# Optimization experiments

Hardware: AMD Instinct MI355X
Metric: run time of the kernel (lower is better)

Reference implementation:

```python
import jax, jax.numpy as jnp
import numpy as np

FILT, HOP, N_MELS, SR, FMIN, FMAX = 1024, 256, 80, 16000, 0.0, 8000.0
CUTOFF = FILT // 2 + 1  # 513


def _hann_periodic(n):
    t = np.arange(n)
    return 0.5 - 0.5 * np.cos(2.0 * np.pi * t / n)


def _hz_to_mel(f):
    # librosa slaney scale (htk=False)
    f = np.asarray(f, dtype=np.float64)
    f_sp = 200.0 / 3.0
    min_log_hz = 1000.0
    min_log_mel = min_log_hz / f_sp
    logstep = np.log(6.4) / 27.0
    return np.where(f >= min_log_hz,
                    min_log_mel + np.log(np.maximum(f, 1e-10) / min_log_hz) / logstep,
                    f / f_sp)


def _mel_to_hz(m):
    m = np.asarray(m, dtype=np.float64)
    f_sp = 200.0 / 3.0
    min_log_hz = 1000.0
    min_log_mel = min_log_hz / f_sp
    logstep = np.log(6.4) / 27.0
    return np.where(m >= min_log_mel,
                    min_log_hz * np.exp(logstep * (m - min_log_mel)),
                    m * f_sp)


def _mel_filterbank(sr, n_fft, n_mels, fmin, fmax):
    # librosa.filters.mel with norm='slaney', htk=False
    fftfreqs = np.linspace(0.0, sr / 2.0, n_fft // 2 + 1)
    mel_f = _mel_to_hz(np.linspace(_hz_to_mel(fmin), _hz_to_mel(fmax), n_mels + 2))
    fdiff = np.diff(mel_f)
    ramps = mel_f[:, None] - fftfreqs[None, :]
    lower = -ramps[:-2] / fdiff[:-1, None]
    upper = ramps[2:] / fdiff[1:, None]
    weights = np.maximum(0.0, np.minimum(lower, upper))
    enorm = 2.0 / (mel_f[2:n_mels + 2] - mel_f[:n_mels])  # slaney normalization
    weights *= enorm[:, None]
    return weights.astype(np.float32)  # [n_mels, n_fft//2+1]


def _forward_basis(n_fft):
    # windowed real/imag DFT rows, as in STFT.__init__
    fourier = np.fft.fft(np.eye(n_fft))
    basis = np.vstack([fourier[:CUTOFF].real, fourier[:CUTOFF].imag]).astype(np.float32)
    basis *= _hann_periodic(n_fft).astype(np.float32)[None, :]
    return basis  # [2*CUTOFF, n_fft] = [1026, 1024]


def setup_inputs() -> dict:
    key = jax.random.key(0)
    y = jax.random.normal(key, (16, 524288), dtype=jnp.float32)
    forward_basis = jnp.asarray(_forward_basis(FILT))
    mel_basis = jnp.asarray(_mel_filterbank(SR, FILT, N_MELS, FMIN, FMAX))
    return {"y": y, "forward_basis": forward_basis, "mel_basis": mel_basis}


def reference(y, forward_basis, mel_basis):
    # STFT.transform: reflect pad by n_fft//2 then conv1d with DFT basis, stride=hop
    yp = jnp.pad(y, ((0, 0), (FILT // 2, FILT // 2)), mode='reflect')[:, None, :]  # [B,1,T+1024]
    ft = jax.lax.conv_general_dilated(
        yp, forward_basis[:, None, :], window_strides=(HOP,), padding='VALID',
        dimension_numbers=('NCH', 'OIH', 'NCH'))  # [B, 1026, n_frames]
    real, imag = ft[:, :CUTOFF, :], ft[:, CUTOFF:, :]
    magnitude = jnp.sqrt(real * real + imag * imag)  # [B, 513, n_frames]
    mel = jnp.einsum('mf,bft->bmt', mel_basis, magnitude)  # [B, 80, n_frames]
    return jnp.log(jnp.maximum(mel, 1e-5))
```

## Files before the change

kernel.cpp:

```cpp
#include <hip/hip_runtime.h>
#include <math.h>

#define HOP     256
#define CUTOFF  513
#define NMELS   80
#define BATCH   16
#define LEN     524288
#define NFRAMES 2049
#define NFFT    1024
#define KW      48
#define WSTRIDE 49
#define TBLK    16

#define ZIDX(i) ((i) + ((i) >> 4))

__device__ __forceinline__ float2 cmul(float2 a, float2 b) {
    return make_float2(a.x * b.x - a.y * b.y, a.x * b.y + a.y * b.x);
}

__global__ void setup_tables(float* __restrict__ tw, float* __restrict__ win) {
    int i = blockIdx.x * blockDim.x + threadIdx.x;
    if (i < NFFT / 2) {
        double th = -2.0 * M_PI * (double)i / (double)NFFT;
        tw[2 * i]     = (float)cos(th);
        tw[2 * i + 1] = (float)sin(th);
    }
    if (i < NFFT) {
        double th = 2.0 * M_PI * (double)i / (double)NFFT;
        win[i] = (float)(0.5 - 0.5 * cos(th));
    }
}

__global__ __launch_bounds__(256) void mel_pack(const float* __restrict__ melw,
                                                int* __restrict__ kstart,
                                                float* __restrict__ wpack) {
    __shared__ int smin;
    const int m = blockIdx.x;
    if (threadIdx.x == 0) smin = CUTOFF;
    __syncthreads();
    const float* row = melw + m * CUTOFF;
    int local = CUTOFF;
    for (int k = threadIdx.x; k < CUTOFF; k += 256)
        if (row[k] > 0.0f && k < local) local = k;
    atomicMin(&smin, local);
    __syncthreads();
    int ks = smin;
    if (ks >= CUTOFF) ks = 0;
    if (threadIdx.x == 0) kstart[m] = ks;
    for (int j = threadIdx.x; j < KW; j += 256) {
        int k = ks + j;
        wpack[m * KW + j] = (k < CUTOFF) ? row[k] : 0.0f;
    }
}

__global__ __launch_bounds__(256) void stft_mel(const float* __restrict__ y,
                                                const float* __restrict__ tw,
                                                const float* __restrict__ win,
                                                const int* __restrict__ kstart,
                                                const float* __restrict__ wpack,
                                                float* __restrict__ out) {
    __shared__ float2 z[NFFT + NFFT / 16];
    __shared__ float  mag0[576];
    __shared__ float  mag1[576];
    __shared__ float  wl[NMELS * WSTRIDE];
    __shared__ float  melbuf[NMELS][TBLK + 1];
    __shared__ int    ksl[NMELS];
    const int tid   = threadIdx.x;
    const int tbase = blockIdx.x * TBLK;
    const int b     = blockIdx.y;
    const float* yb = y + (size_t)b * LEN;
    const float2* twg = (const float2*)tw;

    float2 w1r[4], w2r[4], w3r[4];
    #pragma unroll
    for (int st = 0; st < 4; ++st) {
        const int L   = 1 << (8 - 2 * st);
        const int s   = 1 << (2 * st);
        const int off = tid & (L - 1);
        float2 wa = twg[off * s];
        float2 wb = twg[2 * off * s];
        w1r[st] = wa; w2r[st] = wb; w3r[st] = cmul(wa, wb);
    }
    float wreg[4];
    #pragma unroll
    for (int q = 0; q < 4; ++q) wreg[q] = win[tid + 256 * q];
    int r4;
    {
        int x = tid, r = 0;
        #pragma unroll
        for (int d4 = 0; d4 < 4; ++d4) { r = (r << 2) | (x & 3); x >>= 2; }
        r4 = r;
    }

    for (int i = tid; i < NMELS * KW; i += 256)
        wl[(i / KW) * WSTRIDE + (i % KW)] = wpack[i];
    if (tid < NMELS) ksl[tid] = kstart[tid];
    if (tid < 63) { mag0[CUTOFF + tid] = 0.0f; mag1[CUTOFF + tid] = 0.0f; }

    #pragma unroll 1
    for (int p = 0; p < TBLK / 2; ++p) {
        const int t0 = tbase + 2 * p;
        const int s0 = t0 * HOP - NFFT / 2;

        float2 e[4];
        #pragma unroll
        for (int q = 0; q < 4; ++q) {
            int praw = s0 + tid + 256 * q;
            int p0 = praw;
            p0 = p0 < 0 ? -p0 : p0;  p0 = p0 >= LEN ? 2 * LEN - 2 - p0 : p0;
            int p1 = praw + HOP;
            p1 = p1 < 0 ? -p1 : p1;  p1 = p1 >= LEN ? 2 * LEN - 2 - p1 : p1;
            e[q] = make_float2(wreg[q] * yb[p0], wreg[q] * yb[p1]);
        }
        {
            float2 t0v = make_float2(e[0].x + e[2].x, e[0].y + e[2].y);
            float2 t1v = make_float2(e[0].x - e[2].x, e[0].y - e[2].y);
            float2 t2v = make_float2(e[1].x + e[3].x, e[1].y + e[3].y);
            float2 t3v = make_float2(e[1].x - e[3].x, e[1].y - e[3].y);
            float2 mit3 = make_float2(t3v.y, -t3v.x);
            float2 B0 = make_float2(t0v.x + t2v.x,  t0v.y + t2v.y);
            float2 B2 = make_float2(t0v.x - t2v.x,  t0v.y - t2v.y);
            float2 B1 = make_float2(t1v.x + mit3.x, t1v.y + mit3.y);
            float2 B3 = make_float2(t1v.x - mit3.x, t1v.y - mit3.y);
            z[ZIDX(tid)]        = B0;
            z[ZIDX(tid + 256)]  = cmul(B1, w1r[0]);
            z[ZIDX(tid + 512)]  = cmul(B2, w2r[0]);
            z[ZIDX(tid + 768)]  = cmul(B3, w3r[0]);
        }
        __syncthreads();

        #pragma unroll
        for (int st = 1; st < 4; ++st) {
            const int L   = 1 << (8 - 2 * st);
            const int off = tid & (L - 1);
            const int i0  = ((tid & ~(L - 1)) << 2) | off;

            float2 a  = z[ZIDX(i0)];
            float2 bb = z[ZIDX(i0 + L)];
            float2 c  = z[ZIDX(i0 + 2 * L)];
            float2 d  = z[ZIDX(i0 + 3 * L)];

            float2 t0v = make_float2(a.x + c.x,  a.y + c.y);
            float2 t1v = make_float2(a.x - c.x,  a.y - c.y);
            float2 t2v = make_float2(bb.x + d.x, bb.y + d.y);
            float2 t3v = make_float2(bb.x - d.x, bb.y - d.y);
            float2 mit3 = make_float2(t3v.y, -t3v.x);

            float2 B0 = make_float2(t0v.x + t2v.x,  t0v.y + t2v.y);
            float2 B2 = make_float2(t0v.x - t2v.x,  t0v.y - t2v.y);
            float2 B1 = make_float2(t1v.x + mit3.x, t1v.y + mit3.y);
            float2 B3 = make_float2(t1v.x - mit3.x, t1v.y - mit3.y);

            z[ZIDX(i0)]         = B0;
            z[ZIDX(i0 + L)]     = cmul(B1, w1r[st]);
            z[ZIDX(i0 + 2 * L)] = cmul(B2, w2r[st]);
            z[ZIDX(i0 + 3 * L)] = cmul(B3, w3r[st]);
            __syncthreads();
        }

        {
            const int i0 = tid * 4;
            float2 a  = z[ZIDX(i0)];
            float2 bb = z[ZIDX(i0 + 1)];
            float2 c  = z[ZIDX(i0 + 2)];
            float2 d  = z[ZIDX(i0 + 3)];

            float2 t0v = make_float2(a.x + c.x,  a.y + c.y);
            float2 t1v = make_float2(a.x - c.x,  a.y - c.y);
            float2 t2v = make_float2(bb.x + d.x, bb.y + d.y);
            float2 t3v = make_float2(bb.x - d.x, bb.y - d.y);
            float2 mit3 = make_float2(t3v.y, -t3v.x);

            float2 B0 = make_float2(t0v.x + t2v.x,  t0v.y + t2v.y);
            float2 B2 = make_float2(t0v.x - t2v.x,  t0v.y - t2v.y);
            float2 B1 = make_float2(t1v.x + mit3.x, t1v.y + mit3.y);
            float2 B3 = make_float2(t1v.x - mit3.x, t1v.y - mit3.y);

            __syncthreads();
            z[ZIDX(r4)]        = B0;
            z[ZIDX(r4 + 256)]  = B1;
            z[ZIDX(r4 + 512)]  = B2;
            z[ZIDX(r4 + 768)]  = B3;
            __syncthreads();
        }

        for (int k = tid; k <= NFFT / 2; k += 256) {
            int nk = (NFFT - k) & (NFFT - 1);
            float2 Zk = z[ZIDX(k)], Zn = z[ZIDX(nk)];
            float f0r = 0.5f * (Zk.x + Zn.x);
            float f0i = 0.5f * (Zk.y - Zn.y);
            float f1r = 0.5f * (Zk.y + Zn.y);
            float f1i = 0.5f * (Zn.x - Zk.x);
            mag0[k] = sqrtf(f0r * f0r + f0i * f0i);
            mag1[k] = sqrtf(f1r * f1r + f1i * f1i);
        }
        __syncthreads();

        if (tid < NMELS) {
            const int m = tid;
            const float* wrow = &wl[m * WSTRIDE];
            const int ks = ksl[m];
            const float* m0 = &mag0[ks];
            const float* m1 = &mag1[ks];
            float acc0 = 0.0f, acc1 = 0.0f;
            #pragma unroll
            for (int j = 0; j < KW; ++j) {
                float w = wrow[j];
                acc0 += w * m0[j];
                acc1 += w * m1[j];
            }
            melbuf[m][2 * p]     = logf(fmaxf(acc0, 1e-5f));
            melbuf[m][2 * p + 1] = logf(fmaxf(acc1, 1e-5f));
        }
    }
    __syncthreads();

    for (int o = tid; o < NMELS * TBLK; o += 256) {
        int m = o >> 4;
        int j = o & (TBLK - 1);
        int t = tbase + j;
        if (t < NFRAMES)
            out[((size_t)b * NMELS + m) * NFRAMES + t] = melbuf[m][j];
    }
}

extern "C" void kernel_launch(void* const* d_in, const int* in_sizes, int n_in,
                              void* d_out, int out_size, void* d_ws, size_t ws_size,
                              hipStream_t stream) {
    const float* y    = (const float*)d_in[0];
    const float* melw = (const float*)d_in[2];
    float* out = (float*)d_out;

    float* tw     = (float*)d_ws;
    float* win    = tw + NFFT;
    int*   kstart = (int*)(win + NFFT);
    float* wpack  = (float*)(kstart + 128);

    setup_tables<<<4, 256, 0, stream>>>(tw, win);
    mel_pack<<<NMELS, 256, 0, stream>>>(melw, kstart, wpack);

    dim3 g((NFRAMES + TBLK - 1) / TBLK, BATCH);
    stft_mel<<<g, 256, 0, stream>>>(y, tw, win, kstart, wpack, out);
}
```

Measured before the change: 173.7 us.

## Prefetch next frame samples, use wave-local LDS fences, shrink mel width

```diff
diff --git a/kernel.cpp b/kernel.cpp
--- a/kernel.cpp
+++ b/kernel.cpp
@@ -8,11 +8,16 @@
 #define LEN     524288
 #define NFRAMES 2049
 #define NFFT    1024
-#define KW      48
-#define WSTRIDE 49
+#define KW      40
+#define WSTRIDE 41
 #define TBLK    16
+#define NPAIRS  (TBLK / 2)
+#define MAGPAD  (CUTOFF + KW - 1)
 
 #define ZIDX(i) ((i) + ((i) >> 4))
+
+#define BARRIER_LDS()    asm volatile("s_waitcnt lgkmcnt(0)\n\ts_barrier" ::: "memory")
+#define FENCE_WAVE_LDS() asm volatile("s_waitcnt lgkmcnt(0)" ::: "memory")
 
 __device__ __forceinline__ float2 cmul(float2 a, float2 b) {
     return make_float2(a.x * b.x - a.y * b.y, a.x * b.y + a.y * b.x);
@@ -60,8 +65,8 @@
                                                 const float* __restrict__ wpack,
                                                 float* __restrict__ out) {
     __shared__ float2 z[NFFT + NFFT / 16];
-    __shared__ float  mag0[576];
-    __shared__ float  mag1[576];
+    __shared__ float  mag0[MAGPAD];
+    __shared__ float  mag1[MAGPAD];
     __shared__ float  wl[NMELS * WSTRIDE];
     __shared__ float  melbuf[NMELS][TBLK + 1];
     __shared__ int    ksl[NMELS];
@@ -83,7 +88,7 @@
     }
     float wreg[4];
     #pragma unroll
-    for (int q = 0; q < 4; ++q) wreg[q] = win[tid + 256 * q];
+    for (int q = 0; q < 4; ++q) wreg[q] = 0.5f * win[tid + 256 * q];
     int r4;
     {
         int x = tid, r = 0;
@@ -95,14 +100,11 @@
     for (int i = tid; i < NMELS * KW; i += 256)
         wl[(i / KW) * WSTRIDE + (i % KW)] = wpack[i];
     if (tid < NMELS) ksl[tid] = kstart[tid];
-    if (tid < 63) { mag0[CUTOFF + tid] = 0.0f; mag1[CUTOFF + tid] = 0.0f; }
-
-    #pragma unroll 1
-    for (int p = 0; p < TBLK / 2; ++p) {
-        const int t0 = tbase + 2 * p;
-        const int s0 = t0 * HOP - NFFT / 2;
-
-        float2 e[4];
+    if (tid < KW - 1) { mag0[CUTOFF + tid] = 0.0f; mag1[CUTOFF + tid] = 0.0f; }
+
+    float pre[8];
+    {
+        const int s0 = tbase * HOP - NFFT / 2;
         #pragma unroll
         for (int q = 0; q < 4; ++q) {
             int praw = s0 + tid + 256 * q;
@@ -110,9 +112,18 @@
             p0 = p0 < 0 ? -p0 : p0;  p0 = p0 >= LEN ? 2 * LEN - 2 - p0 : p0;
             int p1 = praw + HOP;
             p1 = p1 < 0 ? -p1 : p1;  p1 = p1 >= LEN ? 2 * LEN - 2 - p1 : p1;
-            e[q] = make_float2(wreg[q] * yb[p0], wreg[q] * yb[p1]);
-        }
+            pre[2 * q]     = yb[p0];
+            pre[2 * q + 1] = yb[p1];
+        }
+    }
+
+    #pragma unroll 1
+    for (int p = 0; p < NPAIRS; ++p) {
         {
+            float2 e[4];
+            #pragma unroll
+            for (int q = 0; q < 4; ++q)
+                e[q] = make_float2(wreg[q] * pre[2 * q], wreg[q] * pre[2 * q + 1]);
             float2 t0v = make_float2(e[0].x + e[2].x, e[0].y + e[2].y);
             float2 t1v = make_float2(e[0].x - e[2].x, e[0].y - e[2].y);
             float2 t2v = make_float2(e[1].x + e[3].x, e[1].y + e[3].y);
@@ -127,7 +138,21 @@
             z[ZIDX(tid + 512)]  = cmul(B2, w2r[0]);
             z[ZIDX(tid + 768)]  = cmul(B3, w3r[0]);
         }
-        __syncthreads();
+        BARRIER_LDS();
+
+        if (p + 1 < NPAIRS) {
+            const int s0n = (tbase + 2 * (p + 1)) * HOP - NFFT / 2;
+            #pragma unroll
+            for (int q = 0; q < 4; ++q) {
+                int praw = s0n + tid + 256 * q;
+                int p0 = praw;
+                p0 = p0 < 0 ? -p0 : p0;  p0 = p0 >= LEN ? 2 * LEN - 2 - p0 : p0;
+                int p1 = praw + HOP;
+                p1 = p1 < 0 ? -p1 : p1;  p1 = p1 >= LEN ? 2 * LEN - 2 - p1 : p1;
+                pre[2 * q]     = yb[p0];
+                pre[2 * q + 1] = yb[p1];
+            }
+        }
 
         #pragma unroll
         for (int st = 1; st < 4; ++st) {
@@ -155,7 +180,7 @@
             z[ZIDX(i0 + L)]     = cmul(B1, w1r[st]);
             z[ZIDX(i0 + 2 * L)] = cmul(B2, w2r[st]);
             z[ZIDX(i0 + 3 * L)] = cmul(B3, w3r[st]);
-            __syncthreads();
+            FENCE_WAVE_LDS();
         }
 
         {
@@ -176,25 +201,25 @@
             float2 B1 = make_float2(t1v.x + mit3.x, t1v.y + mit3.y);
             float2 B3 = make_float2(t1v.x - mit3.x, t1v.y - mit3.y);
 
-            __syncthreads();
+            BARRIER_LDS();
             z[ZIDX(r4)]        = B0;
             z[ZIDX(r4 + 256)]  = B1;
             z[ZIDX(r4 + 512)]  = B2;
             z[ZIDX(r4 + 768)]  = B3;
-            __syncthreads();
+            BARRIER_LDS();
         }
 
         for (int k = tid; k <= NFFT / 2; k += 256) {
             int nk = (NFFT - k) & (NFFT - 1);
             float2 Zk = z[ZIDX(k)], Zn = z[ZIDX(nk)];
-            float f0r = 0.5f * (Zk.x + Zn.x);
-            float f0i = 0.5f * (Zk.y - Zn.y);
-            float f1r = 0.5f * (Zk.y + Zn.y);
-            float f1i = 0.5f * (Zn.x - Zk.x);
+            float f0r = Zk.x + Zn.x;
+            float f0i = Zk.y - Zn.y;
+            float f1r = Zk.y + Zn.y;
+            float f1i = Zn.x - Zk.x;
             mag0[k] = sqrtf(f0r * f0r + f0i * f0i);
             mag1[k] = sqrtf(f1r * f1r + f1i * f1i);
         }
-        __syncthreads();
+        BARRIER_LDS();
 
         if (tid < NMELS) {
             const int m = tid;
@@ -213,7 +238,7 @@
             melbuf[m][2 * p + 1] = logf(fmaxf(acc1, 1e-5f));
         }
     }
-    __syncthreads();
+    BARRIER_LDS();
 
     for (int o = tid; o < NMELS * TBLK; o += 256) {
         int m = o >> 4;
```

After: 163.6 us. 1.06x faster.
